# Optimization experiments

Measured on AMD Instinct MI355X. Metric: run time of the kernel, lower is better.

The kernel has to match this reference:

```python
import jax, jax.numpy as jnp
import numpy as np

B, T, DKQ, DV, EKQ, EV, H, OUT = 8, 2048, 64, 64, 128, 128, 4, 32
FF = 4 * EV
NEG = -1e30  # additive mask value (safe stand-in for -inf)


def _ln(x, g, b, eps=1e-5):
    m = x.mean(-1, keepdims=True)
    var = ((x - m) ** 2).mean(-1, keepdims=True)
    return (x - m) * jax.lax.rsqrt(var + eps) * g + b


def _attn(q, k, v, mask):
    # q,k,v: [n, T, E] -> heads [n, H, T, dh]; NOTE: no 1/sqrt(d) scaling (faithful to source)
    n, t, _ = q.shape
    q = q.reshape(n, t, H, -1).transpose(0, 2, 1, 3)
    k = k.reshape(n, t, H, -1).transpose(0, 2, 1, 3)
    v = v.reshape(n, t, H, -1).transpose(0, 2, 1, 3)
    w = jnp.einsum('bhqd,bhkd->bhqk', q, k) + mask  # [n,H,T,T]
    a = jax.nn.softmax(w, axis=-1)
    o = jnp.einsum('bhqk,bhkd->bhqd', a, v)
    return o.transpose(0, 2, 1, 3).reshape(n, t, -1)


def setup_inputs() -> dict:
    key = jax.random.key(0)
    ks = jax.random.split(key, 32)
    w = lambda k, s: jax.random.normal(k, s, jnp.float32) * 0.02
    DIN_A = DKQ + DV
    return {
        'kq': jax.random.normal(ks[0], (B, T, DKQ), jnp.float32),
        'v': jax.random.normal(ks[1], (B, T, DV), jnp.float32),
        # Layer A (input_dim = DKQ+DV, embed = EV)
        'A_Wk': w(ks[2], (DIN_A, EV)), 'A_bk': jnp.zeros((EV,), jnp.float32),
        'A_Wq': w(ks[3], (DIN_A, EV)), 'A_bq': jnp.zeros((EV,), jnp.float32),
        'A_Wv': w(ks[4], (DIN_A, EV)), 'A_bv': jnp.zeros((EV,), jnp.float32),
        'A_f1W': w(ks[5], (EV, FF)), 'A_f1b': jnp.zeros((FF,), jnp.float32),
        'A_f2W': w(ks[6], (FF, EV)), 'A_f2b': jnp.zeros((EV,), jnp.float32),
        'A_n1g': jnp.ones((EV,), jnp.float32), 'A_n1b': jnp.zeros((EV,), jnp.float32),
        'A_n2g': jnp.ones((EV,), jnp.float32), 'A_n2b': jnp.zeros((EV,), jnp.float32),
        # Layer B (kq -> EKQ, vA -> EV)
        'B_Wk': w(ks[7], (DKQ, EKQ)), 'B_bk': jnp.zeros((EKQ,), jnp.float32),
        'B_Wq': w(ks[8], (DKQ, EKQ)), 'B_bq': jnp.zeros((EKQ,), jnp.float32),
        'B_Wv': w(ks[9], (EV, EV)), 'B_bv': jnp.zeros((EV,), jnp.float32),
        'B_f1W': w(ks[10], (EV, FF)), 'B_f1b': jnp.zeros((FF,), jnp.float32),
        'B_f2W': w(ks[11], (FF, EV)), 'B_f2b': jnp.zeros((EV,), jnp.float32),
        # Output head
        'out_W': w(ks[12], (EV, OUT)), 'out_b': jnp.zeros((OUT,), jnp.float32),
    }


def reference(kq, v, A_Wk, A_bk, A_Wq, A_bq, A_Wv, A_bv, A_f1W, A_f1b, A_f2W, A_f2b,
              A_n1g, A_n1b, A_n2g, A_n2b, B_Wk, B_bk, B_Wq, B_bq, B_Wv, B_bv,
              B_f1W, B_f1b, B_f2W, B_f2b, out_W, out_b):
    n, t, _ = kq.shape
    i = jnp.arange(t)[:, None]
    j = jnp.arange(t)[None, :]
    mask_a = jnp.where(j <= i, 0.0, NEG).astype(jnp.float32)               # causal (diag=1)
    mask_b = jnp.where((j < i) | ((i == 0) & (j == 0)), 0.0, NEG).astype(jnp.float32)  # strict causal + (0,0) exception

    # ---- Layer A ----
    X = jnp.concatenate([kq, v], axis=-1)
    K = X @ A_Wk + A_bk
    Q = X @ A_Wq + A_bq
    V = X @ A_Wv + A_bv
    attn_out = _attn(Q, K, V, mask_a)
    h1 = _ln(V + attn_out, A_n1g, A_n1b)
    ff = jax.nn.gelu(h1 @ A_f1W + A_f1b, approximate=False) @ A_f2W + A_f2b
    vA = _ln(h1 + ff, A_n2g, A_n2b)

    # ---- Layer B (no residuals / norms: values is overwritten in source) ----
    K2 = kq @ B_Wk + B_bk
    Q2 = kq @ B_Wq + B_bq
    V2 = vA @ B_Wv + B_bv
    attn_out2 = _attn(Q2, K2, V2, mask_b)
    ff2 = jax.nn.gelu(attn_out2 @ B_f1W + B_f1b, approximate=False) @ B_f2W + B_f2b

    return ff2 @ out_W + out_b
```

## Files before the change

### kernel.cpp

```cpp
#include <hip/hip_runtime.h>
#include <hip/hip_bf16.h>
#include <type_traits>

#define TSEQ 2048
#define NBATCH 8
#define NROWS (NBATCH*TSEQ)
#define EMB 128
#define NH 4
#define DH 32
#define OUTD 32
#define APLANE (NROWS*EMB)
#define LOG2E 1.44269504088896340736f
#define NPAR 4

typedef short s8v __attribute__((ext_vector_type(8)));
typedef short s4v __attribute__((ext_vector_type(4)));
typedef float f4v __attribute__((ext_vector_type(4)));
typedef float f16v __attribute__((ext_vector_type(16)));
typedef unsigned int u4v __attribute__((ext_vector_type(4)));

__device__ __forceinline__ unsigned short f2bf(float f){
  unsigned int u = __float_as_uint(f);
  unsigned int r = u + 0x7fffu + ((u >> 16) & 1u);
  return (unsigned short)(r >> 16);
}
__device__ __forceinline__ float bf2f(unsigned short u){
  return __uint_as_float(((unsigned int)u) << 16);
}
__device__ __forceinline__ float exp2fast(float x){
#if __has_builtin(__builtin_amdgcn_exp2f)
  return __builtin_amdgcn_exp2f(x);
#else
  return __expf(x * 0.6931471805599453f);
#endif
}

struct WPack {
  const float* src[10];
  int off[10];
  int ntk[10];
  int rowoff[10];
  int nsh[10];
  int kn[10];
};
__global__ __launch_bounds__(256) void prep(WPack p, short* __restrict__ warena,
                                            const float* __restrict__ kq, const float* __restrict__ v,
                                            unsigned short* __restrict__ X){
  int blk = blockIdx.x;
  if (blk < (NROWS*EMB/256)){
    int idx = blk*256 + threadIdx.x;
    int row = idx >> 7, c = idx & 127;
    float val = (c < 64) ? kq[row*64 + c] : v[row*64 + (c-64)];
    unsigned short hi = f2bf(val);
    X[idx]          = hi;
    X[idx + APLANE] = f2bf(val - bf2f(hi));
    return;
  }
  blk -= (NROWS*EMB/256);
  int m = 0;
  #pragma unroll
  for (int i=0;i<10;i++){
    int nb = p.kn[i] >> 8;
    if (blk < nb){ m = i; break; }
    blk -= nb;
  }
  int idx = blk*256 + threadIdx.x;
  float x = p.src[m][idx];
  int nsh = p.nsh[m];
  int n = idx & ((1<<nsh)-1);
  int k = idx >> nsh;
  int K = p.kn[m] >> nsh;
  unsigned short hi = f2bf(x);
  unsigned short lo = f2bf(x - bf2f(hi));
  short* dh = warena + p.off[m] + (size_t)(p.rowoff[m] + n)*K + k;
  dh[0]        = (short)hi;
  dh[p.ntk[m]] = (short)lo;
}

struct GOuts {
  const float* bias[3];
  float* of[3];
  unsigned short* ob[3];
  float scl[3];
};
template<int CT, int NWV>
__global__ __launch_bounds__(NWV*64) void gemm2(
    const unsigned short* __restrict__ A, int aplane, int lda, int K, int niter,
    const short* __restrict__ wt, int NTK,
    GOuts og, int NT, int nseg, int act,
    unsigned short* __restrict__ vtb, int vcol0){
  __shared__ short As[2][2][64*40];
  const int tid  = threadIdx.x;
  const int w    = tid >> 6;
  const int lane = tid & 63;
  const int col  = lane & 15;
  const int quad = lane >> 4;
  const int row0 = blockIdx.x * 64;
  const int cb   = blockIdx.y*(NWV*16*CT) + w*(16*CT) + col;
  const bool two = (aplane != 0);

  f4v acc[4][CT];
  #pragma unroll
  for (int i=0;i<4;i++)
    #pragma unroll
    for (int j=0;j<CT;j++) acc[i][j] = (f4v){0.f,0.f,0.f,0.f};

  using sv = typename std::conditional<NWV==4, s8v, s4v>::type;
  const int ar = (NWV==4) ? (tid >> 2) : (tid >> 3);
  const int ac = (NWV==4) ? ((tid & 3)*8) : ((tid & 7)*4);
  const unsigned short* abase = A + (size_t)(row0 + ar)*lda;

  sv pah, pal;
  pah = *(const sv*)(abase + ac);
  if (two) pal = *(const sv*)(abase + aplane + ac);

  const short* wbase[CT];
  #pragma unroll
  for (int ct=0;ct<CT;ct++) wbase[ct] = wt + (size_t)(cb + ct*16)*K + quad*8;

  for (int i=0;i<niter;i++){
    const int buf = i & 1;
    *(sv*)&As[buf][0][ar*40 + ac] = pah;
    if (two) *(sv*)&As[buf][1][ar*40 + ac] = pal;
    __syncthreads();
    if (i+1 < niter){
      const int kcol = (i+1)*32 + ac;
      pah = *(const sv*)(abase + kcol);
      if (two) pal = *(const sv*)(abase + aplane + kcol);
    }
    s8v bh[CT], bl[CT];
    #pragma unroll
    for (int ct=0;ct<CT;ct++){
      bh[ct] = *(const s8v*)(wbase[ct] + i*32);
      bl[ct] = *(const s8v*)(wbase[ct] + i*32 + NTK);
    }
    #pragma unroll
    for (int rt=0;rt<4;rt++){
      s8v ah = *(const s8v*)&As[buf][0][(rt*16 + col)*40 + quad*8];
      #pragma unroll
      for (int ct=0;ct<CT;ct++)
        acc[rt][ct] = __builtin_amdgcn_mfma_f32_16x16x32_bf16(ah, bh[ct], acc[rt][ct], 0, 0, 0);
      if (two){
        s8v al = *(const s8v*)&As[buf][1][(rt*16 + col)*40 + quad*8];
        #pragma unroll
        for (int ct=0;ct<CT;ct++)
          acc[rt][ct] = __builtin_amdgcn_mfma_f32_16x16x32_bf16(al, bh[ct], acc[rt][ct], 0, 0, 0);
      }
      #pragma unroll
      for (int ct=0;ct<CT;ct++)
        acc[rt][ct] = __builtin_amdgcn_mfma_f32_16x16x32_bf16(ah, bl[ct], acc[rt][ct], 0, 0, 0);
    }
  }

  const int NB = NWV*16*CT;
  const int cb0 = (int)blockIdx.y * NB;
  bool dotr = false;
  if (NWV == 4) dotr = (vtb != nullptr) && (cb0 >= vcol0) && (cb0 < vcol0 + 128);
  short* Lt = &As[0][0][0];
  if (dotr) __syncthreads();

  #pragma unroll
  for (int ct=0;ct<CT;ct++){
    const int cg = cb + ct*16;
    int seg, lcol, ldc;
    if (nseg > 1){ seg = cg >> 7; lcol = cg & 127; ldc = 128; }
    else         { seg = 0; lcol = cg; ldc = NT; }
    const float bv = og.bias[seg][lcol];
    const float sc = og.scl[seg];
    float* of = og.of[seg];
    unsigned short* ob = og.ob[seg];
    #pragma unroll
    for (int rt=0;rt<4;rt++){
      s4v pk;
      #pragma unroll
      for (int r=0;r<4;r++){
        const int row = row0 + rt*16 + quad*4 + r;
        float val = acc[rt][ct][r] + bv;
        if (act == 1) val = 0.5f*val*(1.f + erff(val*0.70710678118654752440f));
        val *= sc;
        if (ob)      ob[(size_t)row*ldc + lcol] = f2bf(val);
        else if (of) of[(size_t)row*ldc + lcol] = val;
        if (dotr) pk[r] = (short)f2bf(val);
      }
      if (dotr)
        *(s4v*)&Lt[(w*(16*CT) + ct*16 + col)*72 + rt*16 + quad*4] = pk;
    }
  }
  if (NWV == 4){
    if (dotr){
      __syncthreads();
      const int b = row0 >> 11, t0 = row0 & 2047;
      #pragma unroll
      for (int it=0; it<2*CT; it++){
        const int cl = it*32 + (tid>>3);
        const int t8 = (tid&7)*8;
        s8v o = *(const s8v*)&Lt[cl*72 + t8];
        const int cr = cb0 + cl - vcol0;
        *(s8v*)(vtb + ((size_t)((b*4 + (cr>>5))*32 + (cr&31)))*2048 + t0 + t8) = o;
      }
    }
  }
}

template<int MODE>
__global__ __launch_bounds__(512) void gemm_f2(
    const unsigned short* __restrict__ A,
    const short* __restrict__ wt, int NTK,
    const float* __restrict__ bias,
    const unsigned short* __restrict__ resid,
    const float* __restrict__ g, const float* __restrict__ bt,
    unsigned short* __restrict__ outp,
    const float* __restrict__ Wo, const float* __restrict__ bo,
    float* __restrict__ outhead){
  __shared__ short As[2][64*40];
  __shared__ float Lf[64*132];
  __shared__ float Ws2[128*32];
  const int tid  = threadIdx.x;
  const int w    = tid >> 6;
  const int lane = tid & 63;
  const int col  = lane & 15;
  const int quad = lane >> 4;
  const int row0 = blockIdx.x * 64;
  const int cg   = w*16 + col;

  if (MODE == 1){
    for (int idx = tid; idx < 128*32; idx += 512) Ws2[idx] = Wo[idx];
  }

  f4v acc[4];
  #pragma unroll
  for (int i=0;i<4;i++) acc[i] = (f4v){0.f,0.f,0.f,0.f};

  const int ar = tid >> 3, ac = (tid & 7)*4;
  const unsigned short* abase = A + (size_t)(row0 + ar)*512;
  s4v pa = *(const s4v*)(abase + ac);
  const short* wb = wt + (size_t)cg*512 + quad*8;

  for (int i=0;i<16;i++){
    const int buf = i & 1;
    *(s4v*)&As[buf][ar*40 + ac] = pa;
    __syncthreads();
    if (i+1 < 16) pa = *(const s4v*)(abase + (i+1)*32 + ac);
    s8v bh = *(const s8v*)(wb + i*32);
    s8v bl = *(const s8v*)(wb + i*32 + NTK);
    #pragma unroll
    for (int rt=0;rt<4;rt++){
      s8v ah = *(const s8v*)&As[buf][(rt*16 + col)*40 + quad*8];
      acc[rt] = __builtin_amdgcn_mfma_f32_16x16x32_bf16(ah, bh, acc[rt], 0, 0, 0);
      acc[rt] = __builtin_amdgcn_mfma_f32_16x16x32_bf16(ah, bl, acc[rt], 0, 0, 0);
    }
  }

  const float bv = bias[cg];
  #pragma unroll
  for (int rt=0;rt<4;rt++){
    #pragma unroll
    for (int r=0;r<4;r++){
      const int row = rt*16 + quad*4 + r;
      Lf[row*132 + cg] = acc[rt][r] + bv;
    }
  }
  __syncthreads();

  if (MODE == 0){
    for (int rr=0; rr<8; rr++){
      const int row = w*8 + rr;
      const size_t gbase = (size_t)(row0 + row)*EMB;
      float x0 = Lf[row*132 + lane]
               + bf2f(resid[gbase+lane])    + bf2f(resid[gbase+lane+APLANE]);
      float x1 = Lf[row*132 + lane + 64]
               + bf2f(resid[gbase+lane+64]) + bf2f(resid[gbase+lane+64+APLANE]);
      float s  = x0 + x1;
      float s2 = x0*x0 + x1*x1;
      #pragma unroll
      for (int off=1; off<64; off<<=1){
        s  += __shfl_xor(s,  off);
        s2 += __shfl_xor(s2, off);
      }
      float mean = s * (1.f/128.f);
      float var  = s2 * (1.f/128.f) - mean*mean;
      float rstd = rsqrtf(var + 1e-5f);
      float y0 = (x0-mean)*rstd*g[lane]    + bt[lane];
      float y1 = (x1-mean)*rstd*g[lane+64] + bt[lane+64];
      unsigned short h0b = f2bf(y0), h1b = f2bf(y1);
      outp[gbase+lane]             = h0b;
      outp[gbase+lane+64]          = h1b;
      outp[gbase+lane+APLANE]      = f2bf(y0 - bf2f(h0b));
      outp[gbase+lane+64+APLANE]   = f2bf(y1 - bf2f(h1b));
    }
  } else {
    const int row = tid >> 3, c0 = (tid & 7)*4;
    f4v a4;
    #pragma unroll
    for (int j=0;j<4;j++) a4[j] = bo[c0+j];
    #pragma unroll 16
    for (int k=0;k<128;k++){
      const float av = Lf[row*132 + k];
      #pragma unroll
      for (int j=0;j<4;j++) a4[j] = fmaf(av, Ws2[k*32 + c0 + j], a4[j]);
    }
    float* op = outhead + (size_t)(row0 + row)*OUTD + c0;
    #pragma unroll
    for (int j=0;j<4;j++) op[j] = a4[j];
  }
}

#define KSTR 40
#define VSTR 72
__device__ __forceinline__ int kswz(int row, int c){ return (row*KSTR + c) ^ (((row>>3)&3)<<3); }
__device__ __forceinline__ int vswz(int row, int c){ return (row*VSTR + c) ^ (((row>>3)&3)<<3); }

__global__ __launch_bounds__(256, 4) void flash5(const unsigned short* __restrict__ Qb,
                                                 const unsigned short* __restrict__ Kb,
                                                 const unsigned short* __restrict__ Vtb,
                                                 float* __restrict__ O, float* __restrict__ L,
                                                 int mode){
  __shared__ short Kt[64*KSTR];
  __shared__ short Vt[32*VSTR];
  const int tid  = threadIdx.x;
  const int w    = tid >> 6;
  const int lane = tid & 63;
  const int q31  = lane & 31;
  const int hi   = lane >> 5;
  const int bh = blockIdx.y;
  const int b = bh >> 2, h = bh & 3;
  const int par = blockIdx.z;
  float* Op = O + (size_t)par*NROWS*EMB;
  float* Lp = L + (size_t)par*NROWS*NH;
  const int kr = tid >> 2, kc8 = (tid & 3)*8;
  const int vd = tid >> 3, vk8 = (tid & 7)*8;

  for (int pass = 0; pass < 2; pass++){
    const int qt = pass ? (int)blockIdx.x : (15 - (int)blockIdx.x);
    const int qbase = qt*128;
    const int qrow  = qbase + w*32 + q31;
    const int jtmax = 2*qt + 1;

    s8v qB0 = *(const s8v*)(Qb + (size_t)(b*TSEQ + qrow)*EMB + h*DH + hi*8);
    s8v qB1 = *(const s8v*)(Qb + (size_t)(b*TSEQ + qrow)*EMB + h*DH + 16 + hi*8);
    f16v o;
    #pragma unroll
    for (int r=0;r<16;r++) o[r] = 0.f;
    float lr = 0.f;

    if (par <= jtmax){
      s8v ka = *(const s8v*)(Kb + (size_t)(b*TSEQ + par*64 + kr)*EMB + h*DH + kc8);
      s8v va = *(const s8v*)(Vtb + ((size_t)bh*32 + vd)*TSEQ + par*64 + vk8);
      for (int jt = par; jt <= jtmax; jt += NPAR){
        __syncthreads();
        *(s8v*)&Kt[kswz(kr, kc8)] = ka;
        *(s8v*)&Vt[vswz(vd, vk8)] = va;
        __syncthreads();
        if (jt + NPAR <= jtmax){
          ka = *(const s8v*)(Kb + (size_t)(b*TSEQ + (jt+NPAR)*64 + kr)*EMB + h*DH + kc8);
          va = *(const s8v*)(Vtb + ((size_t)bh*32 + vd)*TSEQ + (jt+NPAR)*64 + vk8);
        }
        const bool domask = (jt >= 2*qt);
        #pragma unroll
        for (int kt=0;kt<2;kt++){
          f16v s;
          #pragma unroll
          for (int r=0;r<16;r++) s[r] = 0.f;
          {
            s8v kf0 = *(const s8v*)&Kt[kswz(kt*32 + q31, hi*8)];
            s = __builtin_amdgcn_mfma_f32_32x32x16_bf16(kf0, qB0, s, 0, 0, 0);
            s8v kf1 = *(const s8v*)&Kt[kswz(kt*32 + q31, 16 + hi*8)];
            s = __builtin_amdgcn_mfma_f32_32x32x16_bf16(kf1, qB1, s, 0, 0, 0);
          }
          if (domask){
            #pragma unroll
            for (int r=0;r<16;r++){
              const int jg = jt*64 + kt*32 + (r&3) + 8*(r>>2) + 4*hi;
              const bool ok = (mode==0) ? (jg <= qrow) : ((jg < qrow) || (qrow==0 && jg==0));
              s[r] = ok ? s[r] : -1e30f;
            }
          }
          #pragma unroll
          for (int r=0;r<16;r++){ float pv = exp2fast(s[r]); s[r] = pv; lr += pv; }
          unsigned P2[4][2];
          #pragma unroll
          for (int m=0;m<4;m++){
            asm("v_cvt_pk_bf16_f32 %0, %1, %2" : "=v"(P2[m][0]) : "v"(s[4*m+0]), "v"(s[4*m+1]));
            asm("v_cvt_pk_bf16_f32 %0, %1, %2" : "=v"(P2[m][1]) : "v"(s[4*m+2]), "v"(s[4*m+3]));
          }
          #pragma unroll
          for (int kcl=0;kcl<2;kcl++){
            const unsigned own0 = hi ? P2[2*kcl+1][0] : P2[2*kcl][0];
            const unsigned own1 = hi ? P2[2*kcl+1][1] : P2[2*kcl][1];
            const unsigned inv0 = hi ? P2[2*kcl][0]   : P2[2*kcl+1][0];
            const unsigned inv1 = hi ? P2[2*kcl][1]   : P2[2*kcl+1][1];
            const unsigned sx0 = (unsigned)__shfl_xor((int)inv0, 32);
            const unsigned sx1 = (unsigned)__shfl_xor((int)inv1, 32);
            u4v au;
            au[0] = hi ? sx0 : own0;  au[1] = hi ? sx1 : own1;
            au[2] = hi ? own0 : sx0;  au[3] = hi ? own1 : sx1;
            s8v af = __builtin_bit_cast(s8v, au);
            s8v vf = *(const s8v*)&Vt[vswz(q31, kt*32 + kcl*16 + hi*8)];
            o = __builtin_amdgcn_mfma_f32_32x32x16_bf16(af, vf, o, 0, 0, 0);
          }
        }
      }
    }
    const float lt = lr + __shfl_xor(lr, 32);
    #pragma unroll
    for (int r=0;r<16;r++){
      const int ql = (r&3) + 8*(r>>2) + 4*hi;
      Op[(size_t)(b*TSEQ + qbase + w*32 + ql)*EMB + h*DH + q31] = o[r];
    }
    if (hi == 0) Lp[(size_t)(b*TSEQ + qrow)*NH + h] = lt;
  }
}

__global__ __launch_bounds__(256) void combine_ln(const float* __restrict__ O, const float* __restrict__ L,
                                                  const float* __restrict__ Vf,
                                                  const float* __restrict__ g, const float* __restrict__ bt,
                                                  unsigned short* __restrict__ outp){
  const int row = blockIdx.x*4 + (threadIdx.x >> 6);
  const int tid = threadIdx.x & 63;
  const size_t base = (size_t)row*EMB;
  const int h0 = tid >> 5, h1i = 2 + (tid >> 5);
  float la = 0.f, lb = 0.f, s0 = 0.f, s1 = 0.f;
  #pragma unroll
  for (int p=0;p<NPAR;p++){
    la += L[(size_t)p*NROWS*NH + (size_t)row*NH + h0];
    lb += L[(size_t)p*NROWS*NH + (size_t)row*NH + h1i];
    s0 += O[(size_t)p*NROWS*EMB + base + tid];
    s1 += O[(size_t)p*NROWS*EMB + base + tid + 64];
  }
  float x0 = Vf[base+tid]    + s0/la;
  float x1 = Vf[base+tid+64] + s1/lb;
  float s  = x0 + x1;
  float s2 = x0*x0 + x1*x1;
  #pragma unroll
  for (int off=1; off<64; off<<=1){
    s  += __shfl_xor(s,  off);
    s2 += __shfl_xor(s2, off);
  }
  float mean = s * (1.f/128.f);
  float var  = s2 * (1.f/128.f) - mean*mean;
  float rstd = rsqrtf(var + 1e-5f);
  float y0 = (x0-mean)*rstd*g[tid]    + bt[tid];
  float y1 = (x1-mean)*rstd*g[tid+64] + bt[tid+64];
  unsigned short h0b = f2bf(y0), h1b = f2bf(y1);
  outp[base+tid]             = h0b;
  outp[base+tid+64]          = h1b;
  outp[base+tid+APLANE]      = f2bf(y0 - bf2f(h0b));
  outp[base+tid+64+APLANE]   = f2bf(y1 - bf2f(h1b));
}

__global__ __launch_bounds__(256) void combine_b(const float* __restrict__ O, const float* __restrict__ L,
                                                 unsigned short* __restrict__ outp){
  const int idx = blockIdx.x*256 + threadIdx.x;
  const int row = idx >> 7, c = idx & 127, h = c >> 5;
  float l = 0.f, ov = 0.f;
  #pragma unroll
  for (int p=0;p<NPAR;p++){
    l  += L[(size_t)p*NROWS*NH + (size_t)row*NH + h];
    ov += O[(size_t)p*NROWS*EMB + idx];
  }
  const float v = ov / l;
  unsigned short hb = f2bf(v);
  outp[idx]          = hb;
  outp[idx + APLANE] = f2bf(v - bf2f(hb));
}

extern "C" void kernel_launch(void* const* d_in, const int* in_sizes, int n_in,
                              void* d_out, int out_size, void* d_ws, size_t ws_size,
                              hipStream_t stream) {
  const float* kq    = (const float*)d_in[0];
  const float* v     = (const float*)d_in[1];
  const float* A_Wk  = (const float*)d_in[2];  const float* A_bk  = (const float*)d_in[3];
  const float* A_Wq  = (const float*)d_in[4];  const float* A_bq  = (const float*)d_in[5];
  const float* A_Wv  = (const float*)d_in[6];  const float* A_bv  = (const float*)d_in[7];
  const float* A_f1W = (const float*)d_in[8];  const float* A_f1b = (const float*)d_in[9];
  const float* A_f2W = (const float*)d_in[10]; const float* A_f2b = (const float*)d_in[11];
  const float* A_n1g = (const float*)d_in[12]; const float* A_n1b = (const float*)d_in[13];
  const float* A_n2g = (const float*)d_in[14]; const float* A_n2b = (const float*)d_in[15];
  const float* B_Wk  = (const float*)d_in[16]; const float* B_bk  = (const float*)d_in[17];
  const float* B_Wq  = (const float*)d_in[18]; const float* B_bq  = (const float*)d_in[19];
  const float* B_Wv  = (const float*)d_in[20]; const float* B_bv  = (const float*)d_in[21];
  const float* B_f1W = (const float*)d_in[22]; const float* B_f1b = (const float*)d_in[23];
  const float* B_f2W = (const float*)d_in[24]; const float* B_f2b = (const float*)d_in[25];
  const float* out_W = (const float*)d_in[26]; const float* out_b = (const float*)d_in[27];
  float* out = (float*)d_out;
  (void)in_sizes; (void)n_in; (void)out_size; (void)ws_size;

  char* ws = (char*)d_ws;
  const size_t MB = 1024*1024;
  short* warena = (short*)ws;
  unsigned short* Xs  = (unsigned short*)(ws + 2*MB);
  unsigned short* Qbf = (unsigned short*)(ws + 10*MB);
  unsigned short* Kbf = (unsigned short*)(ws + 14*MB);
  unsigned short* Vtb = (unsigned short*)(ws + 18*MB);
  float* Vf  = (float*)(ws + 22*MB);
  float* Opar = (float*)(ws + 30*MB);
  float* Lpar = (float*)(ws + 62*MB);
  unsigned short* h1p = (unsigned short*)(ws + 66*MB);
  unsigned short* mid = (unsigned short*)(ws + 74*MB);
  unsigned short* vAp = (unsigned short*)(ws + 90*MB);

  WPack p;
  const float* srcs[10] = {A_Wq,A_Wk,A_Wv,A_f1W,A_f2W,B_Wq,B_Wk,B_Wv,B_f1W,B_f2W};
  int kn[10]     = {16384,16384,16384,65536,65536,8192,8192,16384,65536,65536};
  int nsh[10]    = {7,7,7,9,7,7,7,7,9,7};
  int off[10]    = {0,0,0,98304,229376,360448,360448,393216,425984,557056};
  int ntk[10]    = {49152,49152,49152,65536,65536,16384,16384,16384,65536,65536};
  int rowoff[10] = {0,128,256,0,0,0,128,0,0,0};
  int nblk = 0;
  for (int i=0;i<10;i++){
    p.src[i]=srcs[i]; p.kn[i]=kn[i]; p.nsh[i]=nsh[i];
    p.off[i]=off[i]; p.ntk[i]=ntk[i]; p.rowoff[i]=rowoff[i];
    nblk += kn[i] >> 8;
  }
  prep<<<(NROWS*EMB/256) + nblk, 256, 0, stream>>>(p, warena, kq, v, Xs);

  GOuts oQKVA = {{A_bq,A_bk,A_bv},{nullptr,nullptr,Vf},{Qbf,Kbf,nullptr},{LOG2E,1.f,1.f}};
  GOuts oF1A  = {{A_f1b,nullptr,nullptr},{nullptr,nullptr,nullptr},{mid,nullptr,nullptr},{1.f,1.f,1.f}};
  GOuts oQKB  = {{B_bq,B_bk,nullptr},{nullptr,nullptr,nullptr},{Qbf,Kbf,nullptr},{LOG2E,1.f,1.f}};
  GOuts oVB   = {{B_bv,nullptr,nullptr},{nullptr,nullptr,nullptr},{nullptr,nullptr,nullptr}, {1.f,1.f,1.f}};
  GOuts oF1B  = {{B_f1b,nullptr,nullptr},{nullptr,nullptr,nullptr},{mid,nullptr,nullptr},{1.f,1.f,1.f}};

  gemm2<2,4><<<dim3(256,3), 256, 0, stream>>>(Xs, APLANE, 128, 128, 4, warena + 0,      49152, oQKVA, 384, 3, 0, Vtb, 256);
  flash5<<<dim3(8,32,NPAR), 256, 0, stream>>>(Qbf, Kbf, Vtb, Opar, Lpar, 0);
  combine_ln<<<NROWS/4, 256, 0, stream>>>(Opar, Lpar, Vf, A_n1g, A_n1b, h1p);
  gemm2<2,8><<<dim3(256,2), 512, 0, stream>>>(h1p, APLANE, 128, 128, 4, warena + 98304, 65536, oF1A, 512, 1, 1, nullptr, 0);
  gemm_f2<0><<<256, 512, 0, stream>>>(mid, warena + 229376, 65536, A_f2b,
                                      h1p, A_n2g, A_n2b, vAp, nullptr, nullptr, nullptr);

  gemm2<2,4><<<dim3(256,2), 256, 0, stream>>>(Xs, APLANE, 128, 64, 2,  warena + 360448, 16384, oQKB, 256, 2, 0, nullptr, 0);
  gemm2<1,4><<<dim3(256,2), 256, 0, stream>>>(vAp, APLANE, 128, 128, 4, warena + 393216, 16384, oVB, 128, 1, 0, Vtb, 0);
  flash5<<<dim3(8,32,NPAR), 256, 0, stream>>>(Qbf, Kbf, Vtb, Opar, Lpar, 1);
  combine_b<<<NROWS*128/256, 256, 0, stream>>>(Opar, Lpar, h1p);
  gemm2<2,8><<<dim3(256,2), 512, 0, stream>>>(h1p, APLANE, 128, 128, 4, warena + 425984, 65536, oF1B, 512, 1, 1, nullptr, 0);
  gemm_f2<1><<<256, 512, 0, stream>>>(mid, warena + 557056, 65536, B_f2b,
                                      nullptr, nullptr, nullptr, nullptr, out_W, out_b, out);
}
```

Measured before the change: 286.1 us.

## Fuse attention combine and LayerNorm into the FF1 GEMM; widen small GEMM tiles

Adds gemm_f1, which merges the per-partition flash outputs, applies the residual and LayerNorm for layer A (or just normalizes for layer B), keeps the 32-row bf16 hi/lo A tile in shared memory and runs the FF1 GEMM with GELU directly. This removes the combine_ln/combine_b launches and the round trip of h1 through global memory. For layer B, h1 is no longer written out at all. The layer-B QK and V projection GEMMs move to 8-wave blocks covering all 128 columns per block, so the V-transpose path is generalized to trigger on NB==128. In exchange, each gemm_f1 block re-reads every weight from global with no shared-memory staging, and each block handles only 32 rows.

Measured after the change: 323.0 us. 1.13x slower.

```diff
diff --git a/kernel.cpp b/kernel.cpp
--- a/kernel.cpp
+++ b/kernel.cpp
@@ -154,8 +154,7 @@
 
   const int NB = NWV*16*CT;
   const int cb0 = (int)blockIdx.y * NB;
-  bool dotr = false;
-  if (NWV == 4) dotr = (vtb != nullptr) && (cb0 >= vcol0) && (cb0 < vcol0 + 128);
+  const bool dotr = (NB == 128) && (vtb != nullptr) && (cb0 >= vcol0) && (cb0 < vcol0 + 128);
   short* Lt = &As[0][0][0];
   if (dotr) __syncthreads();
 
@@ -183,20 +182,132 @@
         if (dotr) pk[r] = (short)f2bf(val);
       }
       if (dotr)
-        *(s4v*)&Lt[(w*(16*CT) + ct*16 + col)*72 + rt*16 + quad*4] = pk;
-    }
-  }
-  if (NWV == 4){
-    if (dotr){
-      __syncthreads();
-      const int b = row0 >> 11, t0 = row0 & 2047;
-      #pragma unroll
-      for (int it=0; it<2*CT; it++){
-        const int cl = it*32 + (tid>>3);
-        const int t8 = (tid&7)*8;
-        s8v o = *(const s8v*)&Lt[cl*72 + t8];
-        const int cr = cb0 + cl - vcol0;
-        *(s8v*)(vtb + ((size_t)((b*4 + (cr>>5))*32 + (cr&31)))*2048 + t0 + t8) = o;
+        *(s4v*)&Lt[((cg - cb0))*72 + rt*16 + quad*4] = pk;
+    }
+  }
+  if (dotr){
+    __syncthreads();
+    const int b = row0 >> 11, t0 = row0 & 2047;
+    #pragma unroll
+    for (int it=0; it<2*CT; it++){
+      const int cl = it*(NWV*8) + (tid>>3);
+      const int t8 = (tid&7)*8;
+      s8v o = *(const s8v*)&Lt[cl*72 + t8];
+      const int cr = cb0 + cl - vcol0;
+      *(s8v*)(vtb + ((size_t)((b*4 + (cr>>5))*32 + (cr&31)))*2048 + t0 + t8) = o;
+    }
+  }
+}
+
+template<int MODE>
+__global__ __launch_bounds__(512) void gemm_f1(
+    const float* __restrict__ Opar, const float* __restrict__ Lpar,
+    const float* __restrict__ Vf,
+    const float* __restrict__ g, const float* __restrict__ bt,
+    unsigned short* __restrict__ h1out,
+    const short* __restrict__ wt, int NTK,
+    const float* __restrict__ bias,
+    unsigned short* __restrict__ midp){
+  __shared__ short Af[2][32*136];
+  const int tid  = threadIdx.x;
+  const int w    = tid >> 6;
+  const int lane = tid & 63;
+  const int col  = lane & 15;
+  const int quad = lane >> 4;
+  const int row0 = blockIdx.x * 32;
+
+  {
+    const int h0 = lane >> 5, h1i = 2 + (lane >> 5);
+    for (int rr=0; rr<4; rr++){
+      const int row = w*4 + rr;
+      const size_t base = (size_t)(row0 + row)*EMB;
+      float la=0.f, lb=0.f, s0=0.f, s1=0.f;
+      #pragma unroll
+      for (int p2=0;p2<NPAR;p2++){
+        la += Lpar[(size_t)p2*NROWS*NH + (size_t)(row0+row)*NH + h0];
+        lb += Lpar[(size_t)p2*NROWS*NH + (size_t)(row0+row)*NH + h1i];
+        s0 += Opar[(size_t)p2*NROWS*EMB + base + lane];
+        s1 += Opar[(size_t)p2*NROWS*EMB + base + lane + 64];
+      }
+      float x0 = s0/la, x1 = s1/lb;
+      if (MODE == 0){
+        x0 += Vf[base+lane];
+        x1 += Vf[base+lane+64];
+        float s  = x0 + x1;
+        float s2 = x0*x0 + x1*x1;
+        #pragma unroll
+        for (int off=1; off<64; off<<=1){
+          s  += __shfl_xor(s,  off);
+          s2 += __shfl_xor(s2, off);
+        }
+        float mean = s * (1.f/128.f);
+        float var  = s2 * (1.f/128.f) - mean*mean;
+        float rstd = rsqrtf(var + 1e-5f);
+        x0 = (x0-mean)*rstd*g[lane]    + bt[lane];
+        x1 = (x1-mean)*rstd*g[lane+64] + bt[lane+64];
+      }
+      const unsigned short hb0 = f2bf(x0), hb1 = f2bf(x1);
+      const unsigned short lo0 = f2bf(x0 - bf2f(hb0)), lo1 = f2bf(x1 - bf2f(hb1));
+      Af[0][row*136 + lane]      = (short)hb0;
+      Af[0][row*136 + lane + 64] = (short)hb1;
+      Af[1][row*136 + lane]      = (short)lo0;
+      Af[1][row*136 + lane + 64] = (short)lo1;
+      if (MODE == 0){
+        h1out[base+lane]              = hb0;
+        h1out[base+lane+64]           = hb1;
+        h1out[base+lane+APLANE]       = lo0;
+        h1out[base+lane+64+APLANE]    = lo1;
+      }
+    }
+  }
+  __syncthreads();
+
+  const int cb = w*64 + col;
+  f4v acc[2][4];
+  #pragma unroll
+  for (int i=0;i<2;i++)
+    #pragma unroll
+    for (int j=0;j<4;j++) acc[i][j] = (f4v){0.f,0.f,0.f,0.f};
+
+  const short* wb[4];
+  #pragma unroll
+  for (int ct=0;ct<4;ct++) wb[ct] = wt + (size_t)(cb + ct*16)*128 + quad*8;
+
+  for (int i=0;i<4;i++){
+    s8v bh[4], bl[4];
+    #pragma unroll
+    for (int ct=0;ct<4;ct++){
+      bh[ct] = *(const s8v*)(wb[ct] + i*32);
+      bl[ct] = *(const s8v*)(wb[ct] + i*32 + NTK);
+    }
+    #pragma unroll
+    for (int rt=0;rt<2;rt++){
+      s8v ah = *(const s8v*)&Af[0][(rt*16 + col)*136 + i*32 + quad*8];
+      s8v al = *(const s8v*)&Af[1][(rt*16 + col)*136 + i*32 + quad*8];
+      #pragma unroll
+      for (int ct=0;ct<4;ct++)
+        acc[rt][ct] = __builtin_amdgcn_mfma_f32_16x16x32_bf16(ah, bh[ct], acc[rt][ct], 0, 0, 0);
+      #pragma unroll
+      for (int ct=0;ct<4;ct++)
+        acc[rt][ct] = __builtin_amdgcn_mfma_f32_16x16x32_bf16(al, bh[ct], acc[rt][ct], 0, 0, 0);
+      #pragma unroll
+      for (int ct=0;ct<4;ct++)
+        acc[rt][ct] = __builtin_amdgcn_mfma_f32_16x16x32_bf16(ah, bl[ct], acc[rt][ct], 0, 0, 0);
+    }
+  }
+
+  #pragma unroll
+  for (int ct=0;ct<4;ct++){
+    const int cg = cb + ct*16;
+    const float bv = bias[cg];
+    #pragma unroll
+    for (int rt=0;rt<2;rt++){
+      #pragma unroll
+      for (int r=0;r<4;r++){
+        const int row = row0 + rt*16 + quad*4 + r;
+        float val = acc[rt][ct][r] + bv;
+        val = 0.5f*val*(1.f + erff(val*0.70710678118654752440f));
+        midp[(size_t)row*512 + cg] = f2bf(val);
       }
     }
   }
@@ -411,59 +522,6 @@
   }
 }
 
-__global__ __launch_bounds__(256) void combine_ln(const float* __restrict__ O, const float* __restrict__ L,
-                                                  const float* __restrict__ Vf,
-                                                  const float* __restrict__ g, const float* __restrict__ bt,
-                                                  unsigned short* __restrict__ outp){
-  const int row = blockIdx.x*4 + (threadIdx.x >> 6);
-  const int tid = threadIdx.x & 63;
-  const size_t base = (size_t)row*EMB;
-  const int h0 = tid >> 5, h1i = 2 + (tid >> 5);
-  float la = 0.f, lb = 0.f, s0 = 0.f, s1 = 0.f;
-  #pragma unroll
-  for (int p=0;p<NPAR;p++){
-    la += L[(size_t)p*NROWS*NH + (size_t)row*NH + h0];
-    lb += L[(size_t)p*NROWS*NH + (size_t)row*NH + h1i];
-    s0 += O[(size_t)p*NROWS*EMB + base + tid];
-    s1 += O[(size_t)p*NROWS*EMB + base + tid + 64];
-  }
-  float x0 = Vf[base+tid]    + s0/la;
-  float x1 = Vf[base+tid+64] + s1/lb;
-  float s  = x0 + x1;
-  float s2 = x0*x0 + x1*x1;
-  #pragma unroll
-  for (int off=1; off<64; off<<=1){
-    s  += __shfl_xor(s,  off);
-    s2 += __shfl_xor(s2, off);
-  }
-  float mean = s * (1.f/128.f);
-  float var  = s2 * (1.f/128.f) - mean*mean;
-  float rstd = rsqrtf(var + 1e-5f);
-  float y0 = (x0-mean)*rstd*g[tid]    + bt[tid];
-  float y1 = (x1-mean)*rstd*g[tid+64] + bt[tid+64];
-  unsigned short h0b = f2bf(y0), h1b = f2bf(y1);
-  outp[base+tid]             = h0b;
-  outp[base+tid+64]          = h1b;
-  outp[base+tid+APLANE]      = f2bf(y0 - bf2f(h0b));
-  outp[base+tid+64+APLANE]   = f2bf(y1 - bf2f(h1b));
-}
-
-__global__ __launch_bounds__(256) void combine_b(const float* __restrict__ O, const float* __restrict__ L,
-                                                 unsigned short* __restrict__ outp){
-  const int idx = blockIdx.x*256 + threadIdx.x;
-  const int row = idx >> 7, c = idx & 127, h = c >> 5;
-  float l = 0.f, ov = 0.f;
-  #pragma unroll
-  for (int p=0;p<NPAR;p++){
-    l  += L[(size_t)p*NROWS*NH + (size_t)row*NH + h];
-    ov += O[(size_t)p*NROWS*EMB + idx];
-  }
-  const float v = ov / l;
-  unsigned short hb = f2bf(v);
-  outp[idx]          = hb;
-  outp[idx + APLANE] = f2bf(v - bf2f(hb));
-}
-
 extern "C" void kernel_launch(void* const* d_in, const int* in_sizes, int n_in,
                               void* d_out, int out_size, void* d_ws, size_t ws_size,
                               hipStream_t stream) {
@@ -515,23 +573,21 @@
   prep<<<(NROWS*EMB/256) + nblk, 256, 0, stream>>>(p, warena, kq, v, Xs);
 
   GOuts oQKVA = {{A_bq,A_bk,A_bv},{nullptr,nullptr,Vf},{Qbf,Kbf,nullptr},{LOG2E,1.f,1.f}};
-  GOuts oF1A  = {{A_f1b,nullptr,nullptr},{nullptr,nullptr,nullptr},{mid,nullptr,nullptr},{1.f,1.f,1.f}};
   GOuts oQKB  = {{B_bq,B_bk,nullptr},{nullptr,nullptr,nullptr},{Qbf,Kbf,nullptr},{LOG2E,1.f,1.f}};
-  GOuts oVB   = {{B_bv,nullptr,nullptr},{nullptr,nullptr,nullptr},{nullptr,nullptr,nullptr}, {1.f,1.f,1.f}};
-  GOuts oF1B  = {{B_f1b,nullptr,nullptr},{nullptr,nullptr,nullptr},{mid,nullptr,nullptr},{1.f,1.f,1.f}};
-
-  gemm2<2,4><<<dim3(256,3), 256, 0, stream>>>(Xs, APLANE, 128, 128, 4, warena + 0,      49152, oQKVA, 384, 3, 0, Vtb, 256);
+  GOuts oVB   = {{B_bv,nullptr,nullptr},{nullptr,nullptr,nullptr},{nullptr,nullptr,nullptr},{1.f,1.f,1.f}};
+
+  gemm2<2,4><<<dim3(256,3), 256, 0, stream>>>(Xs, APLANE, 128, 128, 4, warena + 0, 49152, oQKVA, 384, 3, 0, Vtb, 256);
   flash5<<<dim3(8,32,NPAR), 256, 0, stream>>>(Qbf, Kbf, Vtb, Opar, Lpar, 0);
-  combine_ln<<<NROWS/4, 256, 0, stream>>>(Opar, Lpar, Vf, A_n1g, A_n1b, h1p);
-  gemm2<2,8><<<dim3(256,2), 512, 0, stream>>>(h1p, APLANE, 128, 128, 4, warena + 98304, 65536, oF1A, 512, 1, 1, nullptr, 0);
+  gemm_f1<0><<<512, 512, 0, stream>>>(Opar, Lpar, Vf, A_n1g, A_n1b, h1p,
+                                      warena + 98304, 65536, A_f1b, mid);
   gemm_f2<0><<<256, 512, 0, stream>>>(mid, warena + 229376, 65536, A_f2b,
                                       h1p, A_n2g, A_n2b, vAp, nullptr, nullptr, nullptr);
 
-  gemm2<2,4><<<dim3(256,2), 256, 0, stream>>>(Xs, APLANE, 128, 64, 2,  warena + 360448, 16384, oQKB, 256, 2, 0, nullptr, 0);
-  gemm2<1,4><<<dim3(256,2), 256, 0, stream>>>(vAp, APLANE, 128, 128, 4, warena + 393216, 16384, oVB, 128, 1, 0, Vtb, 0);
+  gemm2<2,8><<<dim3(256,1), 512, 0, stream>>>(Xs, APLANE, 128, 64, 2,  warena + 360448, 16384, oQKB, 256, 2, 0, nullptr, 0);
+  gemm2<1,8><<<dim3(256,1), 512, 0, stream>>>(vAp, APLANE, 128, 128, 4, warena + 393216, 16384, oVB, 128, 1, 0, Vtb, 0);
   flash5<<<dim3(8,32,NPAR), 256, 0, stream>>>(Qbf, Kbf, Vtb, Opar, Lpar, 1);
-  combine_b<<<NROWS*128/256, 256, 0, stream>>>(Opar, Lpar, h1p);
-  gemm2<2,8><<<dim3(256,2), 512, 0, stream>>>(h1p, APLANE, 128, 128, 4, warena + 425984, 65536, oF1B, 512, 1, 1, nullptr, 0);
+  gemm_f1<1><<<512, 512, 0, stream>>>(Opar, Lpar, nullptr, nullptr, nullptr, nullptr,
+                                      warena + 425984, 65536, B_f1b, mid);
   gemm_f2<1><<<256, 512, 0, stream>>>(mid, warena + 557056, 65536, B_f2b,
                                       nullptr, nullptr, nullptr, nullptr, out_W, out_b, out);
 }
```
